# Kernel tuning notes

Hardware: AMD Instinct MI355X
Metric: run time of the kernel (lower is better)

Reference implementation:

```python
import jax, jax.numpy as jnp
import numpy as np

KERNEL = (9, 9, 9)  # box-filter window
KSIZE = KERNEL[0] * KERNEL[1] * KERNEL[2]  # 729
GAMMA = 1.0


def _box_sum(x):
    # x: [B, C, D, H, W] -> channel-sum then 9x9x9 sliding-window sum (SAME pad),
    # exactly matching F.conv3d with an all-ones [1, C, 9,9,9] kernel, pad=4.
    s = jnp.sum(x, axis=1, keepdims=True)  # [B,1,D,H,W]
    return jax.lax.reduce_window(
        s, jnp.asarray(0.0, s.dtype), jax.lax.add,
        window_dimensions=(1, 1) + KERNEL,
        window_strides=(1, 1, 1, 1, 1),
        padding='SAME')


def setup_inputs() -> dict:
    key = jax.random.key(0)
    k1, k2, k3 = jax.random.split(key, 3)
    shape = (2, 1, 160, 160, 160)
    return {
        'input': jax.random.normal(k1, shape, dtype=jnp.float32),
        'target': jax.random.normal(k2, shape, dtype=jnp.float32),
        'flow': jax.random.normal(k3, shape, dtype=jnp.float32),
    }


def reference(input, target, flow):
    # normalize target from (-1, 1) to (0, 1)
    target = (target + 1.0) * 0.5
    w = jax.nn.sigmoid(flow) ** GAMMA  # voxel-wise confidence weight

    T_sum = _box_sum(target)
    I_sum = _box_sum(input)
    TT_sum = _box_sum(target * target)
    II_sum = _box_sum(input * input)
    IT_sum = _box_sum(input * target)

    Ihat = I_sum / KSIZE
    That = T_sum / KSIZE
    cross = IT_sum - Ihat * T_sum - That * I_sum + That * Ihat * KSIZE
    T_var = TT_sum - 2.0 * That * T_sum + That * That * KSIZE
    I_var = II_sum - 2.0 * Ihat * I_sum + Ihat * Ihat * KSIZE

    cc = cross * cross * w / (T_var * I_var + 1e-5)
    return -1.0 * jnp.mean(cc)
```

## Files before the change

kernel.cpp:

```cpp
#include <hip/hip_runtime.h>


constexpr int NB = 2;
constexpr int ND = 160;
constexpr int NH = 160;
constexpr int NW = 160;
constexpr int TH = 16;
constexpr int TW = 16;
constexpr int DCHUNK = 32;
constexpr int NDCH = ND / DCHUNK;
constexpr int NPL = DCHUNK + 8;
constexpr int NIT = NPL + 1;
constexpr int TRS = 20;
constexpr int TFS = 24 * TRS + 8;
constexpr int PRS = 16;
constexpr int PFS = 16 * PRS + 8;
constexpr float INV_K = 1.0f / 729.0f;
constexpr double INV_COUNT = 1.0 / (double(NB) * ND * NH * NW);

__device__ __forceinline__ void gld_lds16(const float* g, float* l)
{
    __builtin_amdgcn_global_load_lds(
        (const __attribute__((address_space(1))) void*)g,
        (__attribute__((address_space(3))) void*)l, 16, 0, 0);
}

__device__ __forceinline__ void bar_vm0()
{
    asm volatile("s_waitcnt vmcnt(0) lgkmcnt(0)" ::: "memory");
    __builtin_amdgcn_s_barrier();
    __builtin_amdgcn_sched_barrier(0);
}
__device__ __forceinline__ void bar_ds()
{
    asm volatile("s_waitcnt lgkmcnt(0)" ::: "memory");
    __builtin_amdgcn_s_barrier();
    __builtin_amdgcn_sched_barrier(0);
}

__device__ __forceinline__ void dma_plane(const float* __restrict__ in,
                                          const float* __restrict__ tg,
                                          float* __restrict__ inT,
                                          float* __restrict__ tgT,
                                          int b, int dp, int h0, int w0, int tid)
{
    if (tid < 144) {
        int r = tid / 6;
        int q = tid - r * 6;
        int gh = h0 - 4 + r;
        int gw = w0 - 4 + q * 4;
        int wb = (tid >> 6) * 256;
        if (((unsigned)gh < (unsigned)NH) && ((unsigned)gw < (unsigned)NW)) {
            int base = ((b * ND + dp) * NH + gh) * NW + gw;
            gld_lds16(in + base, inT + wb);
            gld_lds16(tg + base, tgT + wb);
        }
    }
}

__device__ __forceinline__ void dma_flow(const float* __restrict__ fl,
                                         float* __restrict__ flT,
                                         int b, int dout, int h0, int w0, int tid)
{
    if (tid < 64) {
        int gh = h0 + (tid >> 2);
        int gw = w0 + ((tid & 3) << 2);
        int base = ((b * ND + dout) * NH + gh) * NW + gw;
        gld_lds16(fl + base, flT);
    }
}

#define W9SLIDE(EXPR, FI)                                                  \
    {                                                                      \
        float p0 = (EXPR(0)), p1 = (EXPR(1)), p2 = (EXPR(2)),              \
              p3 = (EXPR(3)), p4 = (EXPR(4)), p5 = (EXPR(5)),              \
              p6 = (EXPR(6)), p7 = (EXPR(7)), p8 = (EXPR(8)),              \
              p9 = (EXPR(9)), p10 = (EXPR(10)), p11 = (EXPR(11));          \
        float s = p0 + p1 + p2 + p3 + p4 + p5 + p6 + p7 + p8;              \
        float4 o;                                                          \
        o.x = s; s += p9 - p0;                                             \
        o.y = s; s += p10 - p1;                                            \
        o.z = s; s += p11 - p2;                                            \
        o.w = s;                                                           \
        *reinterpret_cast<float4*>(outp + (FI) * TFS) = o;                 \
    }

__device__ __forceinline__ void step2q(int tid, const float* __restrict__ inT,
                                       const float* __restrict__ tgT,
                                       float* __restrict__ t5)
{
    const int r = tid >> 2, q = tid & 3;
    const float4* ip = reinterpret_cast<const float4*>(inT + r * 24 + 4 * q);
    const float4* tp = reinterpret_cast<const float4*>(tgT + r * 24 + 4 * q);
    const float4 i0 = ip[0], i1 = ip[1], i2 = ip[2];
    const float4 t0 = tp[0], t1 = tp[1], t2 = tp[2];
    const float ia[12] = {i0.x, i0.y, i0.z, i0.w, i1.x, i1.y, i1.z, i1.w,
                          i2.x, i2.y, i2.z, i2.w};
    float ta[12] = {t0.x, t0.y, t0.z, t0.w, t1.x, t1.y, t1.z, t1.w,
                    t2.x, t2.y, t2.z, t2.w};
    #pragma unroll
    for (int j = 0; j < 12; ++j) ta[j] = fmaf(ta[j], 0.5f, 0.5f);
    float* outp = t5 + r * TRS + 4 * q;
    #define E_T(j)  ta[j]
    #define E_I(j)  ia[j]
    #define E_TT(j) (ta[j] * ta[j])
    #define E_II(j) (ia[j] * ia[j])
    #define E_IT(j) (ia[j] * ta[j])
    W9SLIDE(E_T, 0)
    W9SLIDE(E_I, 1)
    W9SLIDE(E_TT, 2)
    W9SLIDE(E_II, 3)
    W9SLIDE(E_IT, 4)
    #undef E_T
    #undef E_I
    #undef E_TT
    #undef E_II
    #undef E_IT
}

__device__ __forceinline__ void hpass(int t, const float* __restrict__ t5,
                                      float* __restrict__ Pbuf)
{
    const int f = t >> 4;
    const int rem = t & 15;
    const int wq = rem >> 2, hs = rem & 3;
    const float* bp = t5 + f * TFS + hs * 4 * TRS + wq * 4;
    float4 r4[12];
    #pragma unroll
    for (int k = 0; k < 12; ++k)
        r4[k] = *reinterpret_cast<const float4*>(bp + k * TRS);
    float sx = r4[0].x, sy = r4[0].y, sz = r4[0].z, sw = r4[0].w;
    #pragma unroll
    for (int k = 1; k < 9; ++k) {
        sx += r4[k].x; sy += r4[k].y; sz += r4[k].z; sw += r4[k].w;
    }
    float* op = Pbuf + f * PFS + hs * 4 * PRS + wq * 4;
    *reinterpret_cast<float4*>(op) = make_float4(sx, sy, sz, sw);
    #pragma unroll
    for (int j = 1; j < 4; ++j) {
        sx += r4[8 + j].x - r4[j - 1].x;
        sy += r4[8 + j].y - r4[j - 1].y;
        sz += r4[8 + j].z - r4[j - 1].z;
        sw += r4[8 + j].w - r4[j - 1].w;
        *reinterpret_cast<float4*>(op + j * PRS) = make_float4(sx, sy, sz, sw);
    }
}

__device__ __forceinline__ float cc_value(const float S[5], float flv)
{
    float wgt = 1.0f / (1.0f + __expf(-flv));
    float Ts = S[0], Is = S[1], TTs = S[2], IIs = S[3], ITs = S[4];
    float Ihat = Is * INV_K;
    float That = Ts * INV_K;
    float cross = ITs - Ihat * Ts - That * Is + That * Ihat * 729.0f;
    float T_var = TTs - 2.0f * That * Ts + That * That * 729.0f;
    float I_var = IIs - 2.0f * Ihat * Is + Ihat * Ihat * 729.0f;
    return cross * cross * wgt / (T_var * I_var + 1e-5f);
}

__global__ void __launch_bounds__(256, 4)
cc3d_main(const float* __restrict__ in, const float* __restrict__ tg,
          const float* __restrict__ fl, double* __restrict__ acc_out)
{
    __shared__ __align__(16) float inT[2][576];
    __shared__ __align__(16) float tgT[2][576];
    __shared__ __align__(16) float tmp5[5 * TFS];
    __shared__ __align__(16) float Pb[2][5 * PFS];
    __shared__ __align__(16) float flT[2][256];
    __shared__ float red[4];

    const int tid = threadIdx.x;
    const int w0 = blockIdx.x * TW;
    const int h0 = blockIdx.y * TH;
    const int bz = blockIdx.z;
    const int b  = bz / NDCH;
    const int d0 = (bz - b * NDCH) * DCHUNK;
    const int hh = tid >> 4, ww = tid & 15;

    float ring[45];
    #pragma unroll
    for (int i = 0; i < 45; ++i) ring[i] = 0.f;
    float S[5] = {0.f, 0.f, 0.f, 0.f, 0.f};
    float acc = 0.f;

    {
        float* ifl = &inT[0][0];
        float* tfl = &tgT[0][0];
        for (int i = tid; i < 1152; i += 256) { ifl[i] = 0.f; tfl[i] = -1.f; }
    }
    __syncthreads();
    dma_plane(in, tg, inT[0], tgT[0], b, max(d0 - 4, 0), h0, w0, tid);

    for (int lb = 0; lb < NIT; lb += 9) {
        #pragma unroll
        for (int li = 0; li < 9; ++li) {
            const int l = lb + li;
            if (l < NIT) {
                bar_vm0();
                {
                    int dpn = d0 + l - 3;
                    dpn = min(max(dpn, 0), ND - 1);
                    dma_plane(in, tg, inT[(l + 1) & 1], tgT[(l + 1) & 1],
                              b, dpn, h0, w0, tid);
                }
                {
                    int dout = d0 + l - 8;
                    dout = min(max(dout, 0), ND - 1);
                    dma_flow(fl, flT[l & 1], b, dout, h0, w0, tid);
                }
                if (tid < 96) step2q(tid, inT[l & 1], tgT[l & 1], tmp5);
                bar_ds();
                if (tid >= 176) hpass(tid - 176, tmp5, Pb[l & 1]);
                if (l >= 1) {
                    const bool vz = ((unsigned)(d0 + l - 5) < (unsigned)ND);
                    const int slot = (li + 8) % 9;
                    const float* pb = Pb[(l - 1) & 1];
                    #pragma unroll
                    for (int f = 0; f < 5; ++f) {
                        float pn = vz ? pb[f * PFS + hh * PRS + ww] : 0.f;
                        S[f] += pn - ring[f * 9 + slot];
                        ring[f * 9 + slot] = pn;
                    }
                    if (l >= 9) {
                        float flv = flT[(l - 1) & 1][tid];
                        acc += cc_value(S, flv);
                    }
                }
            }
        }
    }

    #pragma unroll
    for (int off = 32; off > 0; off >>= 1) acc += __shfl_down(acc, off);
    if ((tid & 63) == 0) red[tid >> 6] = acc;
    __syncthreads();
    if (tid == 0) {
        double v = (double)red[0] + (double)red[1] + (double)red[2] + (double)red[3];
        atomicAdd(acc_out, v);
    }
}

__global__ void cc3d_finalize(const double* __restrict__ acc, float* __restrict__ out)
{
    out[0] = (float)(-(acc[0] * INV_COUNT));
}

extern "C" void kernel_launch(void* const* d_in, const int* in_sizes, int n_in,
                              void* d_out, int out_size, void* d_ws, size_t ws_size,
                              hipStream_t stream)
{
    const float* in = (const float*)d_in[0];
    const float* tg = (const float*)d_in[1];
    const float* fl = (const float*)d_in[2];
    float* out = (float*)d_out;
    double* acc = (double*)d_ws;

    hipMemsetAsync(d_ws, 0, sizeof(double), stream);

    dim3 grid(NW / TW, NH / TH, NB * NDCH);
    cc3d_main<<<grid, dim3(256), 0, stream>>>(in, tg, fl, acc);
    cc3d_finalize<<<1, 1, 0, stream>>>(acc, out);
}
```

Measured before the change: 177.3 us.

## Load flow directly into registers and skip redundant edge plane DMAs

Replaces the LDS staging of the flow plane with a direct per-thread global load into a register, software-pipelined one iteration ahead, which removes the flow LDS buffer. Plane DMAs for out-of-range depths and past the last needed plane are now skipped instead of clamped and reloaded. The sched_barrier hints after the barriers are removed so the compiler can schedule across them. Skipping the edge loads relies on the padded LDS contents staying correct, and the register flow load now waits behind the per-iteration vmcnt(0) barrier.

```diff
diff --git a/kernel.cpp b/kernel.cpp
--- a/kernel.cpp
+++ b/kernel.cpp
@@ -29,13 +29,11 @@
 {
     asm volatile("s_waitcnt vmcnt(0) lgkmcnt(0)" ::: "memory");
     __builtin_amdgcn_s_barrier();
-    __builtin_amdgcn_sched_barrier(0);
 }
 __device__ __forceinline__ void bar_ds()
 {
     asm volatile("s_waitcnt lgkmcnt(0)" ::: "memory");
     __builtin_amdgcn_s_barrier();
-    __builtin_amdgcn_sched_barrier(0);
 }
 
 __device__ __forceinline__ void dma_plane(const float* __restrict__ in,
@@ -55,18 +53,6 @@
             gld_lds16(in + base, inT + wb);
             gld_lds16(tg + base, tgT + wb);
         }
-    }
-}
-
-__device__ __forceinline__ void dma_flow(const float* __restrict__ fl,
-                                         float* __restrict__ flT,
-                                         int b, int dout, int h0, int w0, int tid)
-{
-    if (tid < 64) {
-        int gh = h0 + (tid >> 2);
-        int gw = w0 + ((tid & 3) << 2);
-        int base = ((b * ND + dout) * NH + gh) * NW + gw;
-        gld_lds16(fl + base, flT);
     }
 }
 
@@ -166,7 +152,6 @@
     __shared__ __align__(16) float tgT[2][576];
     __shared__ __align__(16) float tmp5[5 * TFS];
     __shared__ __align__(16) float Pb[2][5 * PFS];
-    __shared__ __align__(16) float flT[2][256];
     __shared__ float red[4];
 
     const int tid = threadIdx.x;
@@ -182,6 +167,7 @@
     for (int i = 0; i < 45; ++i) ring[i] = 0.f;
     float S[5] = {0.f, 0.f, 0.f, 0.f, 0.f};
     float acc = 0.f;
+    float flv = 0.f, flv_next = 0.f;
 
     {
         float* ifl = &inT[0][0];
@@ -189,7 +175,7 @@
         for (int i = tid; i < 1152; i += 256) { ifl[i] = 0.f; tfl[i] = -1.f; }
     }
     __syncthreads();
-    dma_plane(in, tg, inT[0], tgT[0], b, max(d0 - 4, 0), h0, w0, tid);
+    if (d0 - 4 >= 0) dma_plane(in, tg, inT[0], tgT[0], b, d0 - 4, h0, w0, tid);
 
     for (int lb = 0; lb < NIT; lb += 9) {
         #pragma unroll
@@ -198,15 +184,14 @@
             if (l < NIT) {
                 bar_vm0();
                 {
-                    int dpn = d0 + l - 3;
-                    dpn = min(max(dpn, 0), ND - 1);
-                    dma_plane(in, tg, inT[(l + 1) & 1], tgT[(l + 1) & 1],
-                              b, dpn, h0, w0, tid);
+                    const int dpn = d0 + l - 3;
+                    if (l + 1 < NPL && (unsigned)dpn < (unsigned)ND)
+                        dma_plane(in, tg, inT[(l + 1) & 1], tgT[(l + 1) & 1],
+                                  b, dpn, h0, w0, tid);
                 }
-                {
-                    int dout = d0 + l - 8;
-                    dout = min(max(dout, 0), ND - 1);
-                    dma_flow(fl, flT[l & 1], b, dout, h0, w0, tid);
+                if (l >= 8 && l < 40) {
+                    const int dout = d0 + l - 8;
+                    flv_next = fl[((b * ND + dout) * NH + (h0 + hh)) * NW + (w0 + ww)];
                 }
                 if (tid < 96) step2q(tid, inT[l & 1], tgT[l & 1], tmp5);
                 bar_ds();
@@ -221,11 +206,9 @@
                         S[f] += pn - ring[f * 9 + slot];
                         ring[f * 9 + slot] = pn;
                     }
-                    if (l >= 9) {
-                        float flv = flT[(l - 1) & 1][tid];
-                        acc += cc_value(S, flv);
-                    }
+                    if (l >= 9) acc += cc_value(S, flv);
                 }
+                flv = flv_next;
             }
         }
     }
```

New measurement: 175.2 us. About the same (-1.2%).
